# Kernel tuning notes

Measured on AMD Instinct MI355X. Metric: run time of the kernel, lower is better.

## Reference

```python
import jax, jax.numpy as jnp
import numpy as np

V, D, DU, H = 50000, 256, 1024, 128
TEMP = 0.01

def time_cosine_emb(t, d_model):
    half = d_model // 2
    div_term = jnp.exp(jnp.arange(half, dtype=jnp.float32) * (-np.log(10000.0) / half))
    scaled = t[..., None] * div_term  # (B, L, half)
    return jnp.concatenate([jnp.sin(scaled), jnp.cos(scaled)], axis=-1)

def setup_inputs() -> dict:
    key = jax.random.key(0)
    ks = jax.random.split(key, 12)
    B, L = 64, 2048
    q_seq = jax.random.randint(ks[0], (B, L), 0, V)
    r_seq = jax.random.randint(ks[1], (B, L), 0, 3)
    t_seq = jax.random.uniform(ks[2], (B, L), dtype=jnp.float32) * 1000.0
    mask = jnp.ones((B, L), dtype=jnp.float32)
    q_tab = jax.random.normal(ks[3], (V, D), dtype=jnp.float32) * 0.02
    q_tab = q_tab.at[0].set(0.0)  # padding_idx=0
    r_tab = jax.random.normal(ks[4], (3, D), dtype=jnp.float32) * 0.02
    r_tab = r_tab.at[0].set(0.0)  # padding_idx=0
    virtual_node = jax.random.normal(ks[5], (1, D), dtype=jnp.float32)
    Ws1 = jax.random.normal(ks[6], (H, 2 * D), dtype=jnp.float32) * (1.0 / np.sqrt(2 * D))
    bs1 = jnp.zeros((H,), dtype=jnp.float32)
    Ws2 = jax.random.normal(ks[7], (1, H), dtype=jnp.float32) * (1.0 / np.sqrt(H))
    bs2 = jnp.zeros((1,), dtype=jnp.float32)
    Wa = jax.random.normal(ks[8], (DU, D), dtype=jnp.float32) * (1.0 / np.sqrt(D))
    ba = jnp.zeros((DU,), dtype=jnp.float32)
    return {"q_seq": q_seq, "r_seq": r_seq, "t_seq": t_seq, "mask": mask,
            "q_tab": q_tab, "r_tab": r_tab, "virtual_node": virtual_node,
            "Ws1": Ws1, "bs1": bs1, "Ws2": Ws2, "bs2": bs2, "Wa": Wa, "ba": ba}

def reference(q_seq, r_seq, t_seq, mask, q_tab, r_tab, virtual_node, Ws1, bs1, Ws2, bs2, Wa, ba):
    B, L = q_seq.shape
    d_model = q_tab.shape[1]
    # embedding gathers + trig time embedding
    h_events = q_tab[q_seq] + r_tab[r_seq] + time_cosine_emb(t_seq, d_model)  # (B,L,D)
    h_virtual = jnp.broadcast_to(virtual_node[None, :, :], (B, L, d_model))
    pair = jnp.concatenate([h_events, h_virtual], axis=-1)  # (B,L,2D)
    # struct_head: Linear -> LeakyReLU(0.2) -> Linear
    hdn = jax.nn.leaky_relu(jnp.einsum('bld,hd->blh', pair, Ws1) + bs1, 0.2)
    logits = jnp.einsum('blh,oh->blo', hdn, Ws2) + bs2  # (B,L,1)
    A_hat = jax.nn.sigmoid(logits / TEMP) * mask[..., None]
    # aggregator: Linear -> LeakyReLU(0.2)
    h_trans = jax.nn.leaky_relu(jnp.einsum('bld,ud->blu', h_events, Wa) + ba, 0.2)  # (B,L,DU)
    u_i = jnp.sum(h_trans * A_hat, axis=1)  # (B,DU)
    return (u_i, jnp.squeeze(A_hat, -1))
```

## Files before the change

### kernel.cpp

```cpp
#include <hip/hip_runtime.h>

typedef unsigned short ushort_t;
typedef unsigned int uint_t;

typedef short bf16x8 __attribute__((ext_vector_type(8)));
typedef float f32x4 __attribute__((ext_vector_type(4)));

#define MFMA16(a, b, c) __builtin_amdgcn_mfma_f32_16x16x32_bf16(a, b, c, 0, 0, 0)

__device__ __forceinline__ ushort_t f2bf(float f) {
    uint_t u = __float_as_uint(f);
    u += 0x7fffu + ((u >> 16) & 1u);
    return (ushort_t)(u >> 16);
}
__device__ __forceinline__ float bf2f(ushort_t h) {
    return __uint_as_float(((uint_t)h) << 16);
}

__global__ void k_prep(const float* __restrict__ Ws1, const float* __restrict__ bs1,
                       const float* __restrict__ virt, const float* __restrict__ Wa,
                       float* __restrict__ consth, ushort_t* __restrict__ wa_b,
                       ushort_t* __restrict__ ws1h, ushort_t* __restrict__ ws1l,
                       float* __restrict__ u_i) {
    int b = blockIdx.x;
    if (b == 0) {
        __shared__ float sred[256];
        int t = threadIdx.x;
        int h = t & 127, half = t >> 7;
        const float* row = Ws1 + h * 512 + 256 + half * 128;
        const float* vv = virt + half * 128;
        float s = 0.f;
#pragma unroll 4
        for (int d = 0; d < 128; ++d) s += row[d] * vv[d];
        sred[t] = s;
        __syncthreads();
        if (t < 128) consth[t] = bs1[t] + sred[t] + sred[t + 128];
        return;
    }
    if (b >= 145) {
        int t = (b - 145) * 1024 + threadIdx.x * 4;
        float4 z = {0.f, 0.f, 0.f, 0.f};
        *(float4*)(u_i + t) = z;
        return;
    }
    const float* src;
    int src_stride, tid;
    ushort_t *dhi, *dlo;
    if (b <= 128) {
        tid = (b - 1) * 256 + threadIdx.x;
        src = Wa; src_stride = 256; dhi = wa_b; dlo = nullptr;
    } else {
        tid = (b - 129) * 256 + threadIdx.x;
        src = Ws1; src_stride = 512; dhi = ws1h; dlo = ws1l;
    }
    int pl = tid & 15, kc = (tid >> 4) & 31, pt = tid >> 9;
    int row = pt * 16 + pl;
    const float* s = src + (size_t)row * src_stride + kc * 8;
    ushort_t hs[8], ls[8];
#pragma unroll
    for (int j = 0; j < 8; ++j) {
        float v = s[j];
        ushort_t h = f2bf(v);
        hs[j] = h;
        ls[j] = f2bf(v - bf2f(h));
    }
    uint4 hv;
    hv.x = hs[0] | ((uint_t)hs[1] << 16); hv.y = hs[2] | ((uint_t)hs[3] << 16);
    hv.z = hs[4] | ((uint_t)hs[5] << 16); hv.w = hs[6] | ((uint_t)hs[7] << 16);
    *(uint4*)(dhi + (size_t)tid * 8) = hv;
    if (dlo) {
        uint4 lv;
        lv.x = ls[0] | ((uint_t)ls[1] << 16); lv.y = ls[2] | ((uint_t)ls[3] << 16);
        lv.z = ls[4] | ((uint_t)ls[5] << 16); lv.w = ls[6] | ((uint_t)ls[7] << 16);
        *(uint4*)(dlo + (size_t)tid * 8) = lv;
    }
}

__global__ __launch_bounds__(256, 2) void k_embed(
    const int* __restrict__ q_seq, const int* __restrict__ r_seq,
    const float* __restrict__ t_seq, const float* __restrict__ q_tab,
    const float* __restrict__ r_tab,
    const ushort_t* __restrict__ ws1h, const ushort_t* __restrict__ ws1l,
    const float* __restrict__ consth, const float* __restrict__ Ws2,
    const float* __restrict__ bs2, const float* __restrict__ mask,
    float* __restrict__ out_ahat, ushort_t* __restrict__ ghi) {
    __shared__ __align__(16) ushort_t sAhi[16384];
    __shared__ __align__(16) ushort_t sAlo[8192];
    __shared__ float sdiv[128];
    __shared__ float sLogit[64];
    int tid = threadIdx.x;
    if (tid < 128) sdiv[tid] = __expf((float)tid * -0.07195578415606394f);
    if (tid < 64) sLogit[tid] = 0.0f;
    int w = tid >> 6, lane = tid & 63;
    int pl = lane & 15, kq = lane >> 4;
    int nl = pl;
    int p0 = blockIdx.x * 64;
    int p = p0 + w * 16 + pl;
    int qv = q_seq[p];
    int rr = r_seq[p];
    float tt = t_seq[p];
    const float* grow = q_tab + (size_t)qv * 256;
    const float* rrow = r_tab + (size_t)rr * 256;
    uint4* gdst = (uint4*)(ghi + (size_t)blockIdx.x * 16384);
    __syncthreads();
    uint4 lo_hold[4];
#pragma unroll
    for (int it = 0; it < 8; ++it) {
        int kc = it * 4 + kq;
        int k0 = kc * 8;
        float4 qa = *(const float4*)(grow + kc * 8);
        float4 qb = *(const float4*)(grow + kc * 8 + 4);
        float4 ra = *(const float4*)(rrow + kc * 8);
        float4 rb = *(const float4*)(rrow + kc * 8 + 4);
        float v[8] = {qa.x + ra.x, qa.y + ra.y, qa.z + ra.z, qa.w + ra.w,
                      qb.x + rb.x, qb.y + rb.y, qb.z + rb.z, qb.w + rb.w};
        bool iscos = (kc >= 16);
#pragma unroll
        for (int j = 0; j < 8; ++j) {
            float ang = tt * sdiv[(k0 + j) & 127];
            v[j] += iscos ? __cosf(ang) : __sinf(ang);
        }
        ushort_t hs[8], ls[8];
#pragma unroll
        for (int j = 0; j < 8; ++j) {
            ushort_t h = f2bf(v[j]);
            hs[j] = h;
            ls[j] = (ushort_t)(__float_as_uint(v[j] - bf2f(h)) >> 16);
        }
        uint4 hv, lv;
        hv.x = hs[0] | ((uint_t)hs[1] << 16); hv.y = hs[2] | ((uint_t)hs[3] << 16);
        hv.z = hs[4] | ((uint_t)hs[5] << 16); hv.w = hs[6] | ((uint_t)hs[7] << 16);
        lv.x = ls[0] | ((uint_t)ls[1] << 16); lv.y = ls[2] | ((uint_t)ls[3] << 16);
        lv.z = ls[4] | ((uint_t)ls[5] << 16); lv.w = ls[6] | ((uint_t)ls[7] << 16);
        int unit = (w * 32 + kc) * 16 + pl;
        *(uint4*)(sAhi + unit * 8) = hv;
        gdst[unit] = hv;
        if (it < 4) {
            *(uint4*)(sAlo + ((w * 16 + kc) * 16 + pl) * 8) = lv;
        } else {
            lo_hold[it - 4] = lv;
        }
    }
    __syncthreads();
    {
        f32x4 acc[4][2];
        f32x4 z4 = {0.f, 0.f, 0.f, 0.f};
#pragma unroll
        for (int mt = 0; mt < 4; ++mt)
#pragma unroll
            for (int nt = 0; nt < 2; ++nt) acc[mt][nt] = z4;
#pragma unroll
        for (int ks = 0; ks < 8; ++ks) {
            if (ks == 4) {
                __syncthreads();
#pragma unroll
                for (int it = 4; it < 8; ++it) {
                    int kc = it * 4 + kq;
                    *(uint4*)(sAlo + ((w * 16 + (kc - 16)) * 16 + pl) * 8) = lo_hold[it - 4];
                }
                __syncthreads();
            }
            bf16x8 bh[2], bl[2];
#pragma unroll
            for (int nt = 0; nt < 2; ++nt) {
                int off = (((w * 2 + nt) * 32 + ks * 4 + kq) * 16 + nl) * 8;
                bh[nt] = *(const bf16x8*)(ws1h + off);
                bl[nt] = *(const bf16x8*)(ws1l + off);
            }
#pragma unroll
            for (int mth = 0; mth < 2; ++mth) {
                bf16x8 ahi[2], alo[2];
#pragma unroll
                for (int mi = 0; mi < 2; ++mi) {
                    int mt = mth * 2 + mi;
                    ahi[mi] = *(const bf16x8*)&sAhi[((mt * 32 + ks * 4 + kq) * 16 + nl) * 8];
                    alo[mi] = *(const bf16x8*)&sAlo[((mt * 16 + (ks & 3) * 4 + kq) * 16 + nl) * 8];
                }
#pragma unroll
                for (int mi = 0; mi < 2; ++mi)
#pragma unroll
                    for (int nt = 0; nt < 2; ++nt) {
                        int mt = mth * 2 + mi;
                        acc[mt][nt] = MFMA16(ahi[mi], bh[nt], acc[mt][nt]);
                        acc[mt][nt] = MFMA16(alo[mi], bh[nt], acc[mt][nt]);
                        acc[mt][nt] = MFMA16(ahi[mi], bl[nt], acc[mt][nt]);
                    }
            }
        }
        float ps[4][4];
#pragma unroll
        for (int mt = 0; mt < 4; ++mt)
#pragma unroll
            for (int r = 0; r < 4; ++r) ps[mt][r] = 0.f;
#pragma unroll
        for (int nt = 0; nt < 2; ++nt) {
            int ng = w * 32 + nt * 16 + nl;
            float chv = consth[ng], w2 = Ws2[ng];
#pragma unroll
            for (int mt = 0; mt < 4; ++mt)
#pragma unroll
                for (int r = 0; r < 4; ++r) {
                    float v = acc[mt][nt][r] + chv;
                    v = fmaxf(v, 0.2f * v);
                    ps[mt][r] += v * w2;
                }
        }
#pragma unroll
        for (int mt = 0; mt < 4; ++mt)
#pragma unroll
            for (int r = 0; r < 4; ++r) {
                float x = ps[mt][r];
                x += __shfl_xor(x, 1, 64);
                x += __shfl_xor(x, 2, 64);
                x += __shfl_xor(x, 4, 64);
                x += __shfl_xor(x, 8, 64);
                ps[mt][r] = x;
            }
        if (nl == 0) {
#pragma unroll
            for (int mt = 0; mt < 4; ++mt)
#pragma unroll
                for (int r = 0; r < 4; ++r)
                    atomicAdd(&sLogit[mt * 16 + kq * 4 + r], ps[mt][r]);
        }
    }
    __syncthreads();
    if (tid < 64) {
        int pp = p0 + tid;
        float lg = sLogit[tid] + bs2[0];
        float y = lg * 100.0f;
        y = fminf(fmaxf(y, -60.f), 60.f);
        float a = 1.0f / (1.0f + expf(-y));
        out_ahat[pp] = a * mask[pp];
    }
}

__global__ __launch_bounds__(256, 2) void k_wa(
    const ushort_t* __restrict__ ghi, const float* __restrict__ out_ahat,
    const ushort_t* __restrict__ wa_b, const float* __restrict__ ba,
    float* __restrict__ u_i) {
    __shared__ __align__(16) ushort_t sA[16384];
    __shared__ float sAh[64];
    int tid = threadIdx.x;
    int p0 = blockIdx.x * 64;
    {
        const uint4* src = (const uint4*)(ghi + (size_t)blockIdx.x * 16384);
        uint4* dst = (uint4*)sA;
#pragma unroll
        for (int i = 0; i < 8; ++i) dst[tid + i * 256] = src[tid + i * 256];
    }
    if (tid < 64) sAh[tid] = out_ahat[p0 + tid];
    __syncthreads();
    int w = tid >> 6, lane = tid & 63;
    int pl = lane & 15, kq = lane >> 4;
    int nl = pl;
    float ah[16];
#pragma unroll
    for (int mt = 0; mt < 4; ++mt)
#pragma unroll
        for (int r = 0; r < 4; ++r) ah[mt * 4 + r] = sAh[mt * 16 + kq * 4 + r];
    int bidx = p0 >> 11;
#pragma unroll 1
    for (int nblk = 0; nblk < 4; ++nblk) {
#pragma unroll 1
        for (int hf = 0; hf < 2; ++hf) {
            const ushort_t* gB = wa_b + (size_t)(w * 16 + nblk * 4 + hf * 2) * 4096 + lane * 8;
            f32x4 acc[4][2];
            bf16x8 bfr[2][2];
#pragma unroll
            for (int nt = 0; nt < 2; ++nt)
                bfr[0][nt] = *(const bf16x8*)(gB + nt * 4096);
#pragma unroll
            for (int ks = 0; ks < 8; ++ks) {
                int cur = ks & 1, nxt = cur ^ 1;
                if (ks < 7) {
#pragma unroll
                    for (int nt = 0; nt < 2; ++nt)
                        bfr[nxt][nt] = *(const bf16x8*)(gB + nt * 4096 + (ks + 1) * 512);
                }
                bf16x8 a_[4];
#pragma unroll
                for (int mt = 0; mt < 4; ++mt)
                    a_[mt] = *(const bf16x8*)&sA[((mt * 32 + ks * 4 + kq) * 16 + nl) * 8];
                if (ks == 0) {
                    f32x4 z4 = {0.f, 0.f, 0.f, 0.f};
#pragma unroll
                    for (int mt = 0; mt < 4; ++mt)
#pragma unroll
                        for (int nt = 0; nt < 2; ++nt)
                            acc[mt][nt] = MFMA16(a_[mt], bfr[0][nt], z4);
                } else {
#pragma unroll
                    for (int mt = 0; mt < 4; ++mt)
#pragma unroll
                        for (int nt = 0; nt < 2; ++nt)
                            acc[mt][nt] = MFMA16(a_[mt], bfr[cur][nt], acc[mt][nt]);
                }
            }
#pragma unroll
            for (int nt = 0; nt < 2; ++nt) {
                int ng = w * 256 + nblk * 64 + (hf * 2 + nt) * 16 + nl;
                float ban = ba[ng];
                float s = 0.f;
#pragma unroll
                for (int mt = 0; mt < 4; ++mt)
#pragma unroll
                    for (int r = 0; r < 4; ++r) {
                        float v = acc[mt][nt][r] + ban;
                        v = fmaxf(v, 0.2f * v);
                        s += v * ah[mt * 4 + r];
                    }
                s += __shfl_xor(s, 16, 64);
                s += __shfl_xor(s, 32, 64);
                if (kq == 0) atomicAdd(&u_i[bidx * 1024 + ng], s);
            }
        }
    }
}

__global__ __launch_bounds__(256, 2) void k_fused_fb(
    const int* __restrict__ q_seq, const int* __restrict__ r_seq,
    const float* __restrict__ t_seq, const float* __restrict__ q_tab,
    const float* __restrict__ r_tab,
    const ushort_t* __restrict__ ws1h, const ushort_t* __restrict__ ws1l,
    const float* __restrict__ consth, const float* __restrict__ Ws2,
    const float* __restrict__ bs2, const float* __restrict__ mask,
    const ushort_t* __restrict__ wa_b, const float* __restrict__ ba,
    float* __restrict__ out_ahat, float* __restrict__ u_i) {
    __shared__ __align__(16) ushort_t sAhi[16384];
    __shared__ __align__(16) ushort_t sAlo[16384];
    __shared__ float sdiv[128];
    __shared__ float sLogit[64];
    __shared__ float sAh[64];
    int tid = threadIdx.x;
    if (tid < 128) sdiv[tid] = __expf((float)tid * -0.07195578415606394f);
    if (tid < 64) sLogit[tid] = 0.0f;
    int w = tid >> 6, lane = tid & 63;
    int pl = lane & 15, kq = lane >> 4;
    int nl = pl;
    int p0 = blockIdx.x * 64;
    int p = p0 + w * 16 + pl;
    int qv = q_seq[p];
    int rr = r_seq[p];
    float tt = t_seq[p];
    const float* grow = q_tab + (size_t)qv * 256;
    const float* rrow = r_tab + (size_t)rr * 256;
    __syncthreads();
#pragma unroll
    for (int it = 0; it < 8; ++it) {
        int kc = it * 4 + kq;
        int k0 = kc * 8;
        float4 qa = *(const float4*)(grow + kc * 8);
        float4 qb = *(const float4*)(grow + kc * 8 + 4);
        float4 ra = *(const float4*)(rrow + kc * 8);
        float4 rb = *(const float4*)(rrow + kc * 8 + 4);
        float v[8] = {qa.x + ra.x, qa.y + ra.y, qa.z + ra.z, qa.w + ra.w,
                      qb.x + rb.x, qb.y + rb.y, qb.z + rb.z, qb.w + rb.w};
        bool iscos = (kc >= 16);
#pragma unroll
        for (int j = 0; j < 8; ++j) {
            float ang = tt * sdiv[(k0 + j) & 127];
            v[j] += iscos ? __cosf(ang) : __sinf(ang);
        }
        ushort_t hs[8], ls[8];
#pragma unroll
        for (int j = 0; j < 8; ++j) {
            ushort_t h = f2bf(v[j]);
            hs[j] = h;
            ls[j] = (ushort_t)(__float_as_uint(v[j] - bf2f(h)) >> 16);
        }
        uint4 hv, lv;
        hv.x = hs[0] | ((uint_t)hs[1] << 16); hv.y = hs[2] | ((uint_t)hs[3] << 16);
        hv.z = hs[4] | ((uint_t)hs[5] << 16); hv.w = hs[6] | ((uint_t)hs[7] << 16);
        lv.x = ls[0] | ((uint_t)ls[1] << 16); lv.y = ls[2] | ((uint_t)ls[3] << 16);
        lv.z = ls[4] | ((uint_t)ls[5] << 16); lv.w = ls[6] | ((uint_t)ls[7] << 16);
        int loff = ((w * 32 + kc) * 16 + pl) * 8;
        *(uint4*)(sAhi + loff) = hv;
        *(uint4*)(sAlo + loff) = lv;
    }
    __syncthreads();
    {
        f32x4 acc[4][2];
        f32x4 z4 = {0.f, 0.f, 0.f, 0.f};
#pragma unroll
        for (int mt = 0; mt < 4; ++mt)
#pragma unroll
            for (int nt = 0; nt < 2; ++nt) acc[mt][nt] = z4;
        bf16x8 bh[2][2], bl[2][2];
#pragma unroll
        for (int nt = 0; nt < 2; ++nt) {
            int off = (((w * 2 + nt) * 32 + kq) * 16 + nl) * 8;
            bh[0][nt] = *(const bf16x8*)(ws1h + off);
            bl[0][nt] = *(const bf16x8*)(ws1l + off);
        }
#pragma unroll
        for (int ks = 0; ks < 8; ++ks) {
            int cur = ks & 1, nxt = cur ^ 1;
            if (ks < 7) {
#pragma unroll
                for (int nt = 0; nt < 2; ++nt) {
                    int off = (((w * 2 + nt) * 32 + (ks + 1) * 4 + kq) * 16 + nl) * 8;
                    bh[nxt][nt] = *(const bf16x8*)(ws1h + off);
                    bl[nxt][nt] = *(const bf16x8*)(ws1l + off);
                }
            }
            bf16x8 ahi[4], alo[4];
#pragma unroll
            for (int mt = 0; mt < 4; ++mt) {
                int off = ((mt * 32 + ks * 4 + kq) * 16 + nl) * 8;
                ahi[mt] = *(const bf16x8*)&sAhi[off];
                alo[mt] = *(const bf16x8*)&sAlo[off];
            }
#pragma unroll
            for (int mt = 0; mt < 4; ++mt)
#pragma unroll
                for (int nt = 0; nt < 2; ++nt) {
                    acc[mt][nt] = MFMA16(ahi[mt], bh[cur][nt], acc[mt][nt]);
                    acc[mt][nt] = MFMA16(alo[mt], bh[cur][nt], acc[mt][nt]);
                    acc[mt][nt] = MFMA16(ahi[mt], bl[cur][nt], acc[mt][nt]);
                }
        }
        float ps[4][4];
#pragma unroll
        for (int mt = 0; mt < 4; ++mt)
#pragma unroll
            for (int r = 0; r < 4; ++r) ps[mt][r] = 0.f;
#pragma unroll
        for (int nt = 0; nt < 2; ++nt) {
            int ng = w * 32 + nt * 16 + nl;
            float chv = consth[ng], w2 = Ws2[ng];
#pragma unroll
            for (int mt = 0; mt < 4; ++mt)
#pragma unroll
                for (int r = 0; r < 4; ++r) {
                    float v = acc[mt][nt][r] + chv;
                    v = fmaxf(v, 0.2f * v);
                    ps[mt][r] += v * w2;
                }
        }
#pragma unroll
        for (int mt = 0; mt < 4; ++mt)
#pragma unroll
            for (int r = 0; r < 4; ++r) {
                float x = ps[mt][r];
                x += __shfl_xor(x, 1, 64);
                x += __shfl_xor(x, 2, 64);
                x += __shfl_xor(x, 4, 64);
                x += __shfl_xor(x, 8, 64);
                ps[mt][r] = x;
            }
        if (nl == 0) {
#pragma unroll
            for (int mt = 0; mt < 4; ++mt)
#pragma unroll
                for (int r = 0; r < 4; ++r)
                    atomicAdd(&sLogit[mt * 16 + kq * 4 + r], ps[mt][r]);
        }
    }
    __syncthreads();
    if (tid < 64) {
        int pp = p0 + tid;
        float lg = sLogit[tid] + bs2[0];
        float y = lg * 100.0f;
        y = fminf(fmaxf(y, -60.f), 60.f);
        float a = 1.0f / (1.0f + expf(-y));
        float av = a * mask[pp];
        out_ahat[pp] = av;
        sAh[tid] = av;
    }
    __syncthreads();
    {
        float ah[16];
#pragma unroll
        for (int mt = 0; mt < 4; ++mt)
#pragma unroll
            for (int r = 0; r < 4; ++r) ah[mt * 4 + r] = sAh[mt * 16 + kq * 4 + r];
        int bidx = p0 >> 11;
#pragma unroll 1
        for (int nblk = 0; nblk < 4; ++nblk) {
#pragma unroll 1
            for (int hf = 0; hf < 2; ++hf) {
                const ushort_t* gB = wa_b + (size_t)(w * 16 + nblk * 4 + hf * 2) * 4096 + lane * 8;
                f32x4 acc[4][2];
                bf16x8 bfr[2][2];
#pragma unroll
                for (int nt = 0; nt < 2; ++nt)
                    bfr[0][nt] = *(const bf16x8*)(gB + nt * 4096);
#pragma unroll
                for (int ks = 0; ks < 8; ++ks) {
                    int cur = ks & 1, nxt = cur ^ 1;
                    if (ks < 7) {
#pragma unroll
                        for (int nt = 0; nt < 2; ++nt)
                            bfr[nxt][nt] = *(const bf16x8*)(gB + nt * 4096 + (ks + 1) * 512);
                    }
                    bf16x8 a_[4];
#pragma unroll
                    for (int mt = 0; mt < 4; ++mt)
                        a_[mt] = *(const bf16x8*)&sAhi[((mt * 32 + ks * 4 + kq) * 16 + nl) * 8];
                    if (ks == 0) {
                        f32x4 z4 = {0.f, 0.f, 0.f, 0.f};
#pragma unroll
                        for (int mt = 0; mt < 4; ++mt)
#pragma unroll
                            for (int nt = 0; nt < 2; ++nt)
                                acc[mt][nt] = MFMA16(a_[mt], bfr[0][nt], z4);
                    } else {
#pragma unroll
                        for (int mt = 0; mt < 4; ++mt)
#pragma unroll
                            for (int nt = 0; nt < 2; ++nt)
                                acc[mt][nt] = MFMA16(a_[mt], bfr[cur][nt], acc[mt][nt]);
                    }
                }
#pragma unroll
                for (int nt = 0; nt < 2; ++nt) {
                    int ng = w * 256 + nblk * 64 + (hf * 2 + nt) * 16 + nl;
                    float ban = ba[ng];
                    float s = 0.f;
#pragma unroll
                    for (int mt = 0; mt < 4; ++mt)
#pragma unroll
                        for (int r = 0; r < 4; ++r) {
                            float v = acc[mt][nt][r] + ban;
                            v = fmaxf(v, 0.2f * v);
                            s += v * ah[mt * 4 + r];
                        }
                    s += __shfl_xor(s, 16, 64);
                    s += __shfl_xor(s, 32, 64);
                    if (kq == 0) atomicAdd(&u_i[bidx * 1024 + ng], s);
                }
            }
        }
    }
}

extern "C" void kernel_launch(void* const* d_in, const int* in_sizes, int n_in,
                              void* d_out, int out_size, void* d_ws, size_t ws_size,
                              hipStream_t stream) {
    const int* q_seq = (const int*)d_in[0];
    const int* r_seq = (const int*)d_in[1];
    const float* t_seq = (const float*)d_in[2];
    const float* mask = (const float*)d_in[3];
    const float* q_tab = (const float*)d_in[4];
    const float* r_tab = (const float*)d_in[5];
    const float* virt = (const float*)d_in[6];
    const float* Ws1 = (const float*)d_in[7];
    const float* bs1 = (const float*)d_in[8];
    const float* Ws2 = (const float*)d_in[9];
    const float* bs2 = (const float*)d_in[10];
    const float* Wa = (const float*)d_in[11];
    const float* ba = (const float*)d_in[12];
    float* out = (float*)d_out;

    ushort_t* wa_b = (ushort_t*)d_ws;
    ushort_t* ws1h = wa_b + 262144;
    ushort_t* ws1l = ws1h + 32768;
    float* ch = (float*)(ws1l + 32768);
    ushort_t* ghi = (ushort_t*)(ch + 128);
    const size_t need = 524288 + 65536 + 65536 + 512 + 67108864;

    hipLaunchKernelGGL(k_prep, dim3(209), dim3(256), 0, stream,
                       Ws1, bs1, virt, Wa, ch, wa_b, ws1h, ws1l, out);
    if (ws_size >= need) {
        hipLaunchKernelGGL(k_embed, dim3(2048), dim3(256), 0, stream,
                           q_seq, r_seq, t_seq, q_tab, r_tab, ws1h, ws1l, ch, Ws2,
                           bs2, mask, out + 65536, ghi);
        hipLaunchKernelGGL(k_wa, dim3(2048), dim3(256), 0, stream,
                           ghi, out + 65536, wa_b, ba, out);
    } else {
        hipLaunchKernelGGL(k_fused_fb, dim3(2048), dim3(256), 0, stream,
                           q_seq, r_seq, t_seq, q_tab, r_tab, ws1h, ws1l, ch, Ws2,
                           bs2, mask, wa_b, ba, out + 65536, out);
    }
}
```

Measured before the change: 242.5 us.

## Hold A fragments in registers in k_wa and prefetch B across passes

k_wa no longer stages the activation tile in LDS. Each wave now loads its full 64x256 bf16 A fragment set (32 bf16x8 vectors) straight from global memory into registers. The nested nblk/hf loops are flattened into 8 passes, and the first B fragments of the next pass are prefetched during the last k-step of the current one. This removes the LDS copy, the LDS reads and the pipeline bubble between passes. The cost is 128 more VGPRs per thread, which may cause spills or lower occupancy under launch_bounds(256,2), and each of the four waves now reads the same A data from global/L2 separately.

```diff
diff --git a/kernel.cpp b/kernel.cpp
--- a/kernel.cpp
+++ b/kernel.cpp
@@ -239,81 +239,80 @@
     const ushort_t* __restrict__ ghi, const float* __restrict__ out_ahat,
     const ushort_t* __restrict__ wa_b, const float* __restrict__ ba,
     float* __restrict__ u_i) {
-    __shared__ __align__(16) ushort_t sA[16384];
     __shared__ float sAh[64];
     int tid = threadIdx.x;
     int p0 = blockIdx.x * 64;
-    {
-        const uint4* src = (const uint4*)(ghi + (size_t)blockIdx.x * 16384);
-        uint4* dst = (uint4*)sA;
-#pragma unroll
-        for (int i = 0; i < 8; ++i) dst[tid + i * 256] = src[tid + i * 256];
-    }
     if (tid < 64) sAh[tid] = out_ahat[p0 + tid];
-    __syncthreads();
     int w = tid >> 6, lane = tid & 63;
-    int pl = lane & 15, kq = lane >> 4;
-    int nl = pl;
+    int kq = lane >> 4, nl = lane & 15;
+    const ushort_t* gA = ghi + (size_t)blockIdx.x * 16384 + lane * 8;
+    bf16x8 afr[4][8];
+#pragma unroll
+    for (int ks = 0; ks < 8; ++ks)
+#pragma unroll
+        for (int mt = 0; mt < 4; ++mt)
+            afr[mt][ks] = *(const bf16x8*)(gA + (mt * 512 + ks * 64) * 8);
+    __syncthreads();
     float ah[16];
 #pragma unroll
     for (int mt = 0; mt < 4; ++mt)
 #pragma unroll
         for (int r = 0; r < 4; ++r) ah[mt * 4 + r] = sAh[mt * 16 + kq * 4 + r];
     int bidx = p0 >> 11;
+    bf16x8 bfr[2][2];
+    {
+        const ushort_t* gB0 = wa_b + (size_t)(w * 16) * 4096 + lane * 8;
+#pragma unroll
+        for (int nt = 0; nt < 2; ++nt)
+            bfr[0][nt] = *(const bf16x8*)(gB0 + nt * 4096);
+    }
 #pragma unroll 1
-    for (int nblk = 0; nblk < 4; ++nblk) {
-#pragma unroll 1
-        for (int hf = 0; hf < 2; ++hf) {
-            const ushort_t* gB = wa_b + (size_t)(w * 16 + nblk * 4 + hf * 2) * 4096 + lane * 8;
-            f32x4 acc[4][2];
-            bf16x8 bfr[2][2];
-#pragma unroll
-            for (int nt = 0; nt < 2; ++nt)
-                bfr[0][nt] = *(const bf16x8*)(gB + nt * 4096);
-#pragma unroll
-            for (int ks = 0; ks < 8; ++ks) {
-                int cur = ks & 1, nxt = cur ^ 1;
-                if (ks < 7) {
+    for (int pass = 0; pass < 8; ++pass) {
+        const ushort_t* gB = wa_b + (size_t)(w * 16 + pass * 2) * 4096 + lane * 8;
+        f32x4 acc[4][2];
+#pragma unroll
+        for (int ks = 0; ks < 8; ++ks) {
+            int cur = ks & 1, nxt = cur ^ 1;
+            if (ks < 7) {
+#pragma unroll
+                for (int nt = 0; nt < 2; ++nt)
+                    bfr[nxt][nt] = *(const bf16x8*)(gB + nt * 4096 + (ks + 1) * 512);
+            } else if (pass < 7) {
+#pragma unroll
+                for (int nt = 0; nt < 2; ++nt)
+                    bfr[nxt][nt] = *(const bf16x8*)(gB + (nt + 2) * 4096);
+            }
+            if (ks == 0) {
+                f32x4 z4 = {0.f, 0.f, 0.f, 0.f};
+#pragma unroll
+                for (int mt = 0; mt < 4; ++mt)
 #pragma unroll
                     for (int nt = 0; nt < 2; ++nt)
-                        bfr[nxt][nt] = *(const bf16x8*)(gB + nt * 4096 + (ks + 1) * 512);
-                }
-                bf16x8 a_[4];
+                        acc[mt][nt] = MFMA16(afr[mt][0], bfr[cur][nt], z4);
+            } else {
 #pragma unroll
                 for (int mt = 0; mt < 4; ++mt)
-                    a_[mt] = *(const bf16x8*)&sA[((mt * 32 + ks * 4 + kq) * 16 + nl) * 8];
-                if (ks == 0) {
-                    f32x4 z4 = {0.f, 0.f, 0.f, 0.f};
-#pragma unroll
-                    for (int mt = 0; mt < 4; ++mt)
-#pragma unroll
-                        for (int nt = 0; nt < 2; ++nt)
-                            acc[mt][nt] = MFMA16(a_[mt], bfr[0][nt], z4);
-                } else {
-#pragma unroll
-                    for (int mt = 0; mt < 4; ++mt)
-#pragma unroll
-                        for (int nt = 0; nt < 2; ++nt)
-                            acc[mt][nt] = MFMA16(a_[mt], bfr[cur][nt], acc[mt][nt]);
-                }
-            }
-#pragma unroll
-            for (int nt = 0; nt < 2; ++nt) {
-                int ng = w * 256 + nblk * 64 + (hf * 2 + nt) * 16 + nl;
-                float ban = ba[ng];
-                float s = 0.f;
-#pragma unroll
-                for (int mt = 0; mt < 4; ++mt)
-#pragma unroll
-                    for (int r = 0; r < 4; ++r) {
-                        float v = acc[mt][nt][r] + ban;
-                        v = fmaxf(v, 0.2f * v);
-                        s += v * ah[mt * 4 + r];
-                    }
-                s += __shfl_xor(s, 16, 64);
-                s += __shfl_xor(s, 32, 64);
-                if (kq == 0) atomicAdd(&u_i[bidx * 1024 + ng], s);
-            }
+#pragma unroll
+                    for (int nt = 0; nt < 2; ++nt)
+                        acc[mt][nt] = MFMA16(afr[mt][ks], bfr[cur][nt], acc[mt][nt]);
+            }
+        }
+#pragma unroll
+        for (int nt = 0; nt < 2; ++nt) {
+            int ng = w * 256 + pass * 32 + nt * 16 + nl;
+            float ban = ba[ng];
+            float s = 0.f;
+#pragma unroll
+            for (int mt = 0; mt < 4; ++mt)
+#pragma unroll
+                for (int r = 0; r < 4; ++r) {
+                    float v = acc[mt][nt][r] + ban;
+                    v = fmaxf(v, 0.2f * v);
+                    s += v * ah[mt * 4 + r];
+                }
+            s += __shfl_xor(s, 16, 64);
+            s += __shfl_xor(s, 32, 64);
+            if (kq == 0) atomicAdd(&u_i[bidx * 1024 + ng], s);
         }
     }
 }
```

After: 256.0 us. 5.6% more time.
